# Optimization experiments

Hardware: AMD Instinct MI355X
Metric: run time of the kernel (lower is better)

Reference implementation:

```python
import jax, jax.numpy as jnp
import numpy as np

N = 30000      # node_size / new_node_size
R = 1000       # rel_size
T = 300000     # triple_size (edges)
D = 128        # node_hid == rel_hid
B = 1024       # train pairs
NNZ = 600000   # nnz of ent_adj / rel_adj
DEPTH = 2
GAMMA = 3.0
EPS = 1e-12    # F.normalize eps


def setup_inputs():
    key = jax.random.key(0)
    ks = jax.random.split(key, 12)
    adj = jnp.stack([jax.random.randint(ks[0], (T,), 0, N),
                     jax.random.randint(ks[1], (T,), 0, N)]).astype(jnp.int64)
    # one relation per triple: row ids are 0..T-1, col ids are relation ids
    r_index = jnp.stack([jnp.arange(T),
                         jax.random.randint(ks[2], (T,), 0, R)]).astype(jnp.int64)
    r_val = jnp.ones((T,), jnp.float32)
    ent_adj = jnp.stack([jax.random.randint(ks[3], (NNZ,), 0, N),
                         jax.random.randint(ks[4], (NNZ,), 0, N)]).astype(jnp.int64)
    rel_adj = jnp.stack([jax.random.randint(ks[5], (NNZ,), 0, N),
                         jax.random.randint(ks[6], (NNZ,), 0, R)]).astype(jnp.int64)
    ent_emb = jax.random.normal(ks[7], (N, D), jnp.float32) * 0.05
    rel_emb = jax.random.normal(ks[8], (R, D), jnp.float32) * 0.05
    attn_e = jax.random.normal(ks[9], (DEPTH, D, 1), jnp.float32) * 0.1
    attn_r = jax.random.normal(ks[10], (DEPTH, D, 1), jnp.float32) * 0.1
    train_pairs = jax.random.randint(ks[11], (B, 2), 0, N).astype(jnp.int64)
    return dict(ent_emb=ent_emb, rel_emb=rel_emb, attn_e=attn_e, attn_r=attn_r,
                r_val=r_val, adj=adj, r_index=r_index, ent_adj=ent_adj,
                rel_adj=rel_adj, train_pairs=train_pairs)


def _segment_softmax(vals, seg, num):
    m = jax.ops.segment_max(vals, seg, num_segments=num)
    e = jnp.exp(vals - m[seg])
    s = jax.ops.segment_sum(e, seg, num_segments=num)
    return e / s[seg]


def _avg(adj, emb):
    # sparse softmax of an all-ones matrix over dim=1 == 1/deg per nonzero, then spmm
    row, col = adj[0], adj[1]
    deg = jax.ops.segment_sum(jnp.ones_like(row, emb.dtype), row, num_segments=N)
    return jax.ops.segment_sum(emb[col] / deg[row][:, None], row, num_segments=N)


def _gat(features, rel_emb, adj, r_index, r_val, kernels):
    features = jnp.tanh(features)
    outputs = [features]
    row, col = adj[0], adj[1]
    for l in range(DEPTH):
        # sparse [T,R] @ rel_emb  -> per-triple relation embedding
        tri_rel = jax.ops.segment_sum(r_val[:, None] * rel_emb[r_index[1]],
                                      r_index[0], num_segments=T)          # [T,D]
        tri_rel = tri_rel / jnp.maximum(
            jnp.linalg.norm(tri_rel, axis=1, keepdims=True), EPS)
        neighs = features[col]                                             # [T,D]
        neighs = neighs - 2.0 * jnp.sum(neighs * tri_rel, axis=1,
                                        keepdims=True) * tri_rel
        att = jnp.squeeze(tri_rel @ kernels[l], axis=-1)                   # [T]
        att = _segment_softmax(att, row, N)
        new_features = jax.ops.segment_sum(neighs * att[:, None], row,
                                           num_segments=N)
        features = jnp.tanh(new_features)
        outputs.append(features)
    return jnp.concatenate(outputs, axis=-1)  # [N, (DEPTH+1)*D]


def _align_loss(pairs, emb):
    l, r = pairs[:, 0], pairs[:, 1]
    l_emb, r_emb = emb[l], emb[r]
    pos = jnp.sum(jnp.square(l_emb - r_emb), axis=-1, keepdims=True)       # [B,1]

    def sqdist(A, Bm):
        return (jnp.sum(jnp.square(A), axis=1)[:, None]
                + jnp.sum(jnp.square(Bm), axis=1)[None, :]
                - 2.0 * A @ Bm.T)

    bi = jnp.arange(pairs.shape[0])
    mask = jnp.ones((pairs.shape[0], N), emb.dtype)
    mask = mask.at[bi, l].add(-1.0).at[bi, r].add(-1.0)  # 1 - onehot(l) - onehot(r)

    def norm_lse(loss):
        mu = jax.lax.stop_gradient(jnp.mean(loss, axis=-1, keepdims=True))
        sd = jax.lax.stop_gradient(jnp.std(loss, axis=-1, keepdims=True))
        loss = (loss - mu) / sd
        return jax.nn.logsumexp(20.0 * loss + 8.0, axis=-1)

    l_loss = norm_lse((pos - sqdist(l_emb, emb) + GAMMA) * mask)
    r_loss = norm_lse((pos - sqdist(r_emb, emb) + GAMMA) * mask)
    return jnp.mean(l_loss + r_loss)


def reference(ent_emb, rel_emb, attn_e, attn_r, r_val, adj, r_index,
              ent_adj, rel_adj, train_pairs):
    ent_feature = _avg(ent_adj, ent_emb)   # [N,D]
    rel_feature = _avg(rel_adj, rel_emb)   # [N,D]
    out_rel = _gat(rel_feature, rel_emb, adj, r_index, r_val, attn_r)
    out_ent = _gat(ent_feature, rel_emb, adj, r_index, r_val, attn_e)
    emb = jnp.concatenate([out_ent, out_rel], axis=-1)  # [N, 6*D]
    return _align_loss(train_pairs, emb)
```

## Files before the change

### kernel.cpp

```cpp
#include <hip/hip_runtime.h>
#include <math.h>

#define N_ENT 30000
#define R_REL 1000
#define T_EDGE 300000
#define B_PAIR 1024
#define NNZ_E 600000
#define GAMMAF 3.0f
#define EPSV 1e-12f
#define EMBD 768
#define NPAD 30720
#define NT128 240
#define PTILES 480
#define SCB 118

typedef _Float16 half8 __attribute__((ext_vector_type(8)));
typedef _Float16 half4v __attribute__((ext_vector_type(4)));
typedef _Float16 half2v __attribute__((ext_vector_type(2)));
typedef float f32x4 __attribute__((ext_vector_type(4)));

__device__ inline void gl_lds16(const _Float16* g, _Float16* l){
  __builtin_amdgcn_global_load_lds(
      (const __attribute__((address_space(1))) unsigned int*)g,
      (__attribute__((address_space(3))) unsigned int*)l, 16, 0, 0);
}

__device__ inline float waveRedSum(float v){
  #pragma unroll
  for(int m=32;m>=1;m>>=1) v += __shfl_xor(v, m, 64);
  return v;
}

__device__ inline float fast_tanh(float x){
  x = fminf(10.f, fmaxf(-10.f, x));
  float e = __expf(2.f*x);
  return (e-1.f)/(e+1.f);
}

__global__ __launch_bounds__(256) void k_prep(const float* __restrict__ ent, const float* __restrict__ rel,
      const float* __restrict__ ae, const float* __restrict__ ar,
      _Float16* ehE, _Float16* ehR, _Float16* Eh, _Float16* relnH, float* expdot,
      const int* __restrict__ rA, int* cA, const int* __restrict__ rE, int* cE,
      const int* __restrict__ rR, int* cR){
  int i = blockIdx.x*256 + threadIdx.x;
  if(i < N_ENT*128) ehE[i] = (_Float16)ent[i];
  if(i < R_REL*128) ehR[i] = (_Float16)rel[i];
  if(i < (NPAD-N_ENT)*EMBD) Eh[(size_t)N_ENT*EMBD + i] = (_Float16)0.f;
  if(i < T_EDGE) atomicAdd(&cA[rA[i]], 1);
  if(i < NNZ_E){ atomicAdd(&cE[rE[i]], 1); atomicAdd(&cR[rR[i]], 1); }
  int r = i >> 6;
  if(r < R_REL){
    int lane = i & 63;
    float2 v = *(const float2*)(rel + (size_t)r*128 + lane*2);
    float ss = waveRedSum(v.x*v.x + v.y*v.y);
    float nrm = fmaxf(sqrtf(ss), EPSV);
    float2 u; u.x = v.x/nrm; u.y = v.y/nrm;
    half2v uh = {(_Float16)u.x, (_Float16)u.y};
    *(half2v*)(relnH + (size_t)r*128 + lane*2) = uh;
    const float* ks[4] = {ae, ae+128, ar, ar+128};
    #pragma unroll
    for(int k=0;k<4;k++){
      float2 w = *(const float2*)(ks[k] + lane*2);
      float d = waveRedSum(u.x*w.x + u.y*w.y);
      if(lane==0) expdot[k*R_REL + r] = __expf(d);
    }
  }
}

__global__ __launch_bounds__(256) void k_scanA(const int* c0, const int* c1, const int* c2,
                                               int* s0, int* s1, int* s2, int* part){
  const int* cnt = blockIdx.y==0 ? c0 : (blockIdx.y==1 ? c1 : c2);
  int* start     = blockIdx.y==0 ? s0 : (blockIdx.y==1 ? s1 : s2);
  __shared__ int wsum[4];
  int i = blockIdx.x*256 + threadIdx.x;
  int lane = threadIdx.x & 63, wid = threadIdx.x >> 6;
  int v = (i < N_ENT) ? cnt[i] : 0;
  int x = v;
  #pragma unroll
  for(int off=1; off<64; off<<=1){ int t=__shfl_up(x,off,64); if(lane>=off) x+=t; }
  if(lane==63) wsum[wid] = x;
  __syncthreads();
  int woff = 0;
  #pragma unroll
  for(int k=0;k<3;k++) if(k < wid) woff += wsum[k];
  if(i < N_ENT) start[i] = woff + x - v;
  if(threadIdx.x == 255) part[blockIdx.y*SCB + blockIdx.x] = woff + x;
}

__global__ __launch_bounds__(256) void k_scanB(int* part, int* tots){
  int wid = threadIdx.x>>6, lane = threadIdx.x&63;
  if(wid >= 3) return;
  int base = wid*SCB;
  int v0 = part[base + lane];
  int i1 = 64 + lane;
  int v1 = (i1 < SCB) ? part[base + i1] : 0;
  int x0 = v0, x1 = v1;
  #pragma unroll
  for(int off=1; off<64; off<<=1){
    int t0=__shfl_up(x0,off,64), t1=__shfl_up(x1,off,64);
    if(lane>=off){ x0+=t0; x1+=t1; }
  }
  int t0 = __shfl(x0, 63, 64);
  int t1 = __shfl(x1, 63, 64);
  part[base + lane] = x0 - v0;
  if(i1 < SCB) part[base + i1] = t0 + x1 - v1;
  if(lane == 0) tots[wid] = t0 + t1;
}

__global__ __launch_bounds__(256) void k_scanC(int* s0, int* s1, int* s2,
                                               int* u0, int* u1, int* u2,
                                               const int* part, const int* tots){
  int y = blockIdx.y;
  int* start  = y==0 ? s0 : (y==1 ? s1 : s2);
  int* cursor = y==0 ? u0 : (y==1 ? u1 : u2);
  int i = blockIdx.x*256 + threadIdx.x;
  int off = part[y*SCB + blockIdx.x];
  if(i < N_ENT){ int v = start[i] + off; start[i] = v; cursor[i] = v; }
  if(i == 0) start[N_ENT] = tots[y];
}

__global__ __launch_bounds__(256) void k_scatter3(
      const int* __restrict__ rA, const int* __restrict__ cAj, const int* __restrict__ rid,
      int* uA, int* scolA, int* sridA,
      const int* __restrict__ rE, const int* __restrict__ cEj, int* uE, int* scolE,
      const int* __restrict__ rR, const int* __restrict__ cRj, int* uR, int* scolR){
  int e = blockIdx.x*256 + threadIdx.x;
  if(e < T_EDGE){
    int p = atomicAdd(&uA[rA[e]], 1);
    scolA[p] = cAj[e];
    sridA[p] = rid[e];
  }
  if(e < NNZ_E){
    int p = atomicAdd(&uE[rE[e]], 1);
    scolE[p] = cEj[e];
    int q = atomicAdd(&uR[rR[e]], 1);
    scolR[q] = cRj[e];
  }
}

__global__ __launch_bounds__(256) void k_avg2(const int* __restrict__ startE, const int* __restrict__ scolE,
                        const _Float16* __restrict__ srcE,
                        const int* __restrict__ startR, const int* __restrict__ scolR,
                        const _Float16* __restrict__ srcR,
                        _Float16* featC, _Float16* Eh){
  int which = blockIdx.y;
  const int* start = which? startR : startE;
  const int* scol  = which? scolR : scolE;
  const _Float16* src = which? srcR : srcE;
  int pairOff = which? 2 : 0;
  int coloff  = which? 384 : 0;
  int r = blockIdx.x*4 + (threadIdx.x>>6);
  int lane = threadIdx.x & 63;
  int s0 = start[r], s1 = start[r+1];
  float ax=0.f, ay=0.f;
  int e = s0;
  for(; e+1<s1; e+=2){
    int c0 = scol[e], c1 = scol[e+1];
    half2v v0 = *(const half2v*)(src + (size_t)c0*128 + lane*2);
    half2v v1 = *(const half2v*)(src + (size_t)c1*128 + lane*2);
    ax += (float)v0[0] + (float)v1[0]; ay += (float)v0[1] + (float)v1[1];
  }
  if(e<s1){
    int c0 = scol[e];
    half2v v0 = *(const half2v*)(src + (size_t)c0*128 + lane*2);
    ax += (float)v0[0]; ay += (float)v0[1];
  }
  float inv = (s1>s0) ? 1.0f/(float)(s1-s0) : 0.f;
  float vx = fast_tanh(ax*inv), vy = fast_tanh(ay*inv);
  half2v hv = {(_Float16)vx, (_Float16)vy};
  *(half2v*)(featC + (size_t)r*256 + lane*4 + pairOff) = hv;
  *(half2v*)(Eh + (size_t)r*EMBD + coloff + lane*2) = hv;
}

__global__ __launch_bounds__(256) void k_edge2(const int* __restrict__ start, const int* __restrict__ scol,
      const int* __restrict__ srid, const _Float16* __restrict__ relnH,
      const float* __restrict__ expE, const float* __restrict__ expR,
      const _Float16* __restrict__ featIn, _Float16* featOut, _Float16* Eh, int colEnt, int colRel){
  int r = blockIdx.x*4 + (threadIdx.x>>6);
  int lane = threadIdx.x & 63;
  int s0 = start[r], s1 = start[r+1];
  float aEx=0,aEy=0,aRx=0,aRy=0, swE=0, swR=0;
  int e = s0;
  for(; e+1<s1; e+=2){
    int c0=scol[e], q0=srid[e], c1=scol[e+1], q1=srid[e+1];
    float wE0=expE[q0], wR0=expR[q0], wE1=expE[q1], wR1=expR[q1];
    half2v u0h = *(const half2v*)(relnH + (size_t)q0*128 + lane*2);
    half2v u1h = *(const half2v*)(relnH + (size_t)q1*128 + lane*2);
    half4v h0 = *(const half4v*)(featIn + (size_t)c0*256 + lane*4);
    half4v h1 = *(const half4v*)(featIn + (size_t)c1*256 + lane*4);
    float u0x=(float)u0h[0], u0y=(float)u0h[1], u1x=(float)u1h[0], u1y=(float)u1h[1];
    float e0x=(float)h0[0], e0y=(float)h0[1], r0x=(float)h0[2], r0y=(float)h0[3];
    float e1x=(float)h1[0], e1y=(float)h1[1], r1x=(float)h1[2], r1y=(float)h1[3];
    float d0 = e0x*u0x + e0y*u0y;
    float d1 = r0x*u0x + r0y*u0y;
    float d2 = e1x*u1x + e1y*u1y;
    float d3 = r1x*u1x + r1y*u1y;
    #pragma unroll
    for(int m=32;m>=1;m>>=1){
      d0 += __shfl_xor(d0,m,64); d1 += __shfl_xor(d1,m,64);
      d2 += __shfl_xor(d2,m,64); d3 += __shfl_xor(d3,m,64);
    }
    aEx += wE0*(e0x - 2.f*d0*u0x) + wE1*(e1x - 2.f*d2*u1x);
    aEy += wE0*(e0y - 2.f*d0*u0y) + wE1*(e1y - 2.f*d2*u1y);
    aRx += wR0*(r0x - 2.f*d1*u0x) + wR1*(r1x - 2.f*d3*u1x);
    aRy += wR0*(r0y - 2.f*d1*u0y) + wR1*(r1y - 2.f*d3*u1y);
    swE += wE0+wE1; swR += wR0+wR1;
  }
  if(e<s1){
    int c0=scol[e], q0=srid[e];
    float wE0=expE[q0], wR0=expR[q0];
    half2v u0h = *(const half2v*)(relnH + (size_t)q0*128 + lane*2);
    half4v h0 = *(const half4v*)(featIn + (size_t)c0*256 + lane*4);
    float u0x=(float)u0h[0], u0y=(float)u0h[1];
    float e0x=(float)h0[0], e0y=(float)h0[1], r0x=(float)h0[2], r0y=(float)h0[3];
    float d0 = e0x*u0x + e0y*u0y;
    float d1 = r0x*u0x + r0y*u0y;
    #pragma unroll
    for(int m=32;m>=1;m>>=1){ d0 += __shfl_xor(d0,m,64); d1 += __shfl_xor(d1,m,64); }
    aEx += wE0*(e0x - 2.f*d0*u0x);
    aEy += wE0*(e0y - 2.f*d0*u0y);
    aRx += wR0*(r0x - 2.f*d1*u0x);
    aRy += wR0*(r0y - 2.f*d1*u0y);
    swE += wE0; swR += wR0;
  }
  float iE = (s1>s0) ? 1.f/swE : 0.f;
  float iR = (s1>s0) ? 1.f/swR : 0.f;
  float vEx = fast_tanh(aEx*iE), vEy = fast_tanh(aEy*iE);
  float vRx = fast_tanh(aRx*iR), vRy = fast_tanh(aRy*iR);
  half4v ov = {(_Float16)vEx,(_Float16)vEy,(_Float16)vRx,(_Float16)vRy};
  *(half4v*)(featOut + (size_t)r*256 + lane*4) = ov;
  half2v he = {(_Float16)vEx,(_Float16)vEy};
  half2v hr = {(_Float16)vRx,(_Float16)vRy};
  *(half2v*)(Eh + (size_t)r*EMBD + colEnt + lane*2) = he;
  *(half2v*)(Eh + (size_t)r*EMBD + colRel + lane*2) = hr;
}

__global__ __launch_bounds__(256) void k_post(const _Float16* __restrict__ Eh, _Float16* embT,
      const int* __restrict__ tp, _Float16* Wh, float* cvec,
      float* qn, float* Svec, float* Pvec, float* QQ){
  __shared__ __align__(16) _Float16 til[64][72];
  __shared__ float sh0[256], sh1[256], sh2[256];
  int b = blockIdx.x;
  int tid = threadIdx.x;
  if(b < 5760){
    int r0 = (b % 480)*64, c0 = (b / 480)*64;
    int rr = tid>>3, c8 = (tid&7)*8;
    #pragma unroll
    for(int p=0;p<2;p++){
      int gr = r0 + rr + p*32;
      uint4 v = make_uint4(0u,0u,0u,0u);
      if(gr < N_ENT) v = *(const uint4*)(Eh + (size_t)gr*EMBD + c0 + c8);
      *(uint4*)&til[rr + p*32][c8] = v;
    }
    __syncthreads();
    #pragma unroll
    for(int p=0;p<2;p++){
      int cc = rr + p*32;
      __align__(16) _Float16 tmp[8];
      #pragma unroll
      for(int j=0;j<8;j++) tmp[j] = til[c8 + j][cc];
      *(uint4*)(embT + (size_t)(c0+cc)*NPAD + r0 + c8) = *(uint4*)tmp;
    }
  } else if(b < 5760 + B_PAIR){
    int i = b - 5760;
    int l = tp[2*i], r = tp[2*i+1];
    float sl=0.f, sr=0.f, sp=0.f;
    for(int c=tid;c<EMBD;c+=256){
      _Float16 lh = Eh[(size_t)l*EMBD+c], rh = Eh[(size_t)r*EMBD+c];
      float le = (float)lh, re = (float)rh;
      Wh[(size_t)i*EMBD+c]=lh; Wh[(size_t)(B_PAIR+i)*EMBD+c]=rh;
      sl += le*le; sr += re*re; float d = le-re; sp += d*d;
    }
    sh0[tid]=sl; sh1[tid]=sr; sh2[tid]=sp;
    __syncthreads();
    for(int w=128;w>0;w>>=1){
      if(tid<w){ sh0[tid]+=sh0[tid+w]; sh1[tid]+=sh1[tid+w]; sh2[tid]+=sh2[tid+w]; }
      __syncthreads();
    }
    if(tid==0){
      float pos = sh2[0];
      cvec[i]        = pos + GAMMAF - sh0[0];
      cvec[B_PAIR+i] = pos + GAMMAF - sh1[0];
    }
  } else {
    int wid = tid>>6, lane = tid&63;
    int gw = (b - 5760 - B_PAIR)*4 + wid;
    float s[12], p[12];
    #pragma unroll
    for(int q=0;q<12;q++){ s[q]=0.f; p[q]=0.f; }
    float q1=0.f, q2=0.f;
    for(int r=gw; r<NPAD; r+=960){
      if(r >= N_ENT){ if(lane==0) qn[r] = 1e30f; continue; }
      float v[12]; float ss=0.f;
      #pragma unroll
      for(int q=0;q<12;q++){ v[q] = (float)Eh[(size_t)r*EMBD + lane + 64*q]; ss += v[q]*v[q]; }
      ss = waveRedSum(ss);
      ss = __shfl(ss, 0, 64);
      if(lane==0){ qn[r] = ss; q1 += ss; q2 += ss*ss; }
      #pragma unroll
      for(int q=0;q<12;q++){ s[q] += v[q]; p[q] += ss*v[q]; }
    }
    #pragma unroll
    for(int q=0;q<12;q++){
      unsafeAtomicAdd(&Svec[lane + 64*q], s[q]);
      unsafeAtomicAdd(&Pvec[lane + 64*q], p[q]);
    }
    if(lane==0){ unsafeAtomicAdd(&QQ[0], q1); unsafeAtomicAdd(&QQ[1], q2); }
  }
}

__global__ __launch_bounds__(256) void k_syrk(const _Float16* __restrict__ embT, float* G){
  __shared__ __align__(16) _Float16 As[128*64];
  __shared__ __align__(16) _Float16 Bs[128*64];
  int id = blockIdx.x;
  int xcd = id & 7, rest = id >> 3;
  int kslc = xcd + 8*(rest/36);
  int tile = rest % 36;
  int m0 = (tile/6)*128, n0 = (tile%6)*128;
  int kbeg = kslc*1920, kend = kbeg + 1920;
  int tid = threadIdx.x;
  int w = tid>>6, lane = tid&63;
  int quad = lane>>4, l15 = lane&15;
  int lr = lane>>3, lc = lane&7;
  int wm = (w>>1)*64, wn = (w&1)*64;
  f32x4 acc[4][4];
  #pragma unroll
  for(int i=0;i<4;i++)
    #pragma unroll
    for(int j=0;j<4;j++) acc[i][j] = (f32x4){0.f,0.f,0.f,0.f};
  for(int k0=kbeg;k0<kend;k0+=64){
    #pragma unroll
    for(int p=0;p<4;p++){
      int r = p*32 + w*8 + lr;
      int cg = lc ^ (r&7);
      gl_lds16(embT + (size_t)(m0+r)*NPAD + k0 + cg*8, As + (p*32 + w*8)*64);
      gl_lds16(embT + (size_t)(n0+r)*NPAD + k0 + cg*8, Bs + (p*32 + w*8)*64);
    }
    __syncthreads();
    #pragma unroll
    for(int ks=0;ks<2;ks++){
      half8 af[4], bf[4];
      #pragma unroll
      for(int i=0;i<4;i++){
        int ml = wm + i*16 + l15;
        af[i] = *(half8*)(As + ml*64 + (((ks<<2)|quad) ^ (ml&7))*8);
      }
      #pragma unroll
      for(int j=0;j<4;j++){
        int nl = wn + j*16 + l15;
        bf[j] = *(half8*)(Bs + nl*64 + (((ks<<2)|quad) ^ (nl&7))*8);
      }
      #pragma unroll
      for(int i=0;i<4;i++)
        #pragma unroll
        for(int j=0;j<4;j++)
          acc[i][j] = __builtin_amdgcn_mfma_f32_16x16x32_f16(af[i], bf[j], acc[i][j], 0,0,0);
    }
    __syncthreads();
  }
  #pragma unroll
  for(int i=0;i<4;i++){
    #pragma unroll
    for(int r=0;r<4;r++){
      int m = m0 + wm + i*16 + quad*4 + r;
      #pragma unroll
      for(int j=0;j<4;j++){
        int n = n0 + wn + j*16 + l15;
        unsafeAtomicAdd(&G[(size_t)m*EMBD + n], acc[i][j][r]);
      }
    }
  }
}

__global__ __launch_bounds__(256) void k_gemmTh(const _Float16* __restrict__ Wh, const float* __restrict__ G,
                                                float* Tm){
  int tid = threadIdx.x, w = tid>>6, lane = tid&63;
  int quad = lane>>4, l15 = lane&15;
  int n0 = blockIdx.x*64;
  #pragma unroll
  for(int half=0; half<2; half++){
    int m0 = (blockIdx.y*8 + half*4 + w)*64;
    f32x4 acc[4][4];
    #pragma unroll
    for(int i=0;i<4;i++)
      #pragma unroll
      for(int j=0;j<4;j++) acc[i][j] = (f32x4){0.f,0.f,0.f,0.f};
    const _Float16* aB[4]; const float* bB[4];
    #pragma unroll
    for(int i=0;i<4;i++){
      aB[i] = Wh + (size_t)(m0+i*16+l15)*EMBD + quad*8;
      bB[i] = G  + (size_t)(n0+i*16+l15)*EMBD + quad*8;
    }
    for(int ks=0; ks<24; ks++){
      half8 af[4], bf[4];
      #pragma unroll
      for(int i=0;i<4;i++) af[i] = *(const half8*)(aB[i] + ks*32);
      #pragma unroll
      for(int j=0;j<4;j++){
        float4 f0 = *(const float4*)(bB[j] + ks*32);
        float4 f1 = *(const float4*)(bB[j] + ks*32 + 4);
        half8 h = {(_Float16)f0.x,(_Float16)f0.y,(_Float16)f0.z,(_Float16)f0.w,
                   (_Float16)f1.x,(_Float16)f1.y,(_Float16)f1.z,(_Float16)f1.w};
        bf[j] = h;
      }
      #pragma unroll
      for(int i=0;i<4;i++)
        #pragma unroll
        for(int j=0;j<4;j++)
          acc[i][j] = __builtin_amdgcn_mfma_f32_16x16x32_f16(af[i], bf[j], acc[i][j], 0,0,0);
    }
    #pragma unroll
    for(int i=0;i<4;i++)
      #pragma unroll
      for(int r=0;r<4;r++){
        int mg = m0 + i*16 + quad*4 + r;
        #pragma unroll
        for(int j=0;j<4;j++)
          Tm[(size_t)mg*EMBD + n0 + j*16 + l15] = acc[i][j][r];
      }
  }
}

__global__ __launch_bounds__(256) void k_rowstats(const _Float16* __restrict__ Wh, const float* __restrict__ Tm,
      const _Float16* __restrict__ Eh, const float* __restrict__ qn, const float* __restrict__ cvec,
      const int* __restrict__ tp, const float* __restrict__ Svec, const float* __restrict__ Pvec,
      const float* __restrict__ QQ, float* alpha, float* betav){
  int row = blockIdx.x*4 + (threadIdx.x>>6);
  int lane = threadIdx.x & 63;
  if(row >= 2*B_PAIR) return;
  int pi = row & (B_PAIR-1);
  int lp = tp[2*pi], rp = tp[2*pi+1];
  float d1=0,d2=0,d3=0,dl=0,dr=0;
  #pragma unroll
  for(int k=0;k<12;k++){
    int d = lane + 64*k;
    float a = (float)Wh[(size_t)row*EMBD + d];
    d1 += a*Svec[d];
    d2 += a*Pvec[d];
    d3 += a*Tm[(size_t)row*EMBD + d];
    dl += a*(float)Eh[(size_t)lp*EMBD + d];
    dr += a*(float)Eh[(size_t)rp*EMBD + d];
  }
  d1=waveRedSum(d1); d2=waveRedSum(d2); d3=waveRedSum(d3);
  dl=waveRedSum(dl); dr=waveRedSum(dr);
  if(lane==0){
    double c = (double)cvec[row], Q = (double)QQ[0], Q2 = (double)QQ[1], Nn = (double)N_ENT;
    double su  = Nn*c - Q + 2.0*(double)d1;
    double su2 = Nn*c*c - 2.0*c*Q + Q2 + 4.0*(c*(double)d1 - (double)d2) + 4.0*(double)d3;
    double ul = c - (double)qn[lp] + 2.0*(double)dl;
    double ur = c - (double)qn[rp] + 2.0*(double)dr;
    su -= ul + ur;
    if(lp != rp) su2 -= ul*ul + ur*ur;
    double mu = su/Nn;
    double var = su2/Nn - mu*mu;
    double sd = sqrt(fmax(var, 0.0));
    double al = 20.0/sd;
    alpha[row] = (float)al;
    betav[row] = (float)(8.0 - al*mu);
  }
}

__device__ inline void lseMerge(float& mx, float& sm, float om, float os){
  if(om > mx){ sm = sm*expf(mx-om) + os; mx = om; }
  else if(om != -INFINITY){ sm += os*expf(om-mx); }
}

__global__ __launch_bounds__(256,3) void k_gemmB(const _Float16* __restrict__ Wh, const _Float16* __restrict__ Eh,
    const float* __restrict__ cvec, const float* __restrict__ qn, const int* __restrict__ tp,
    const float* __restrict__ alpha, const float* __restrict__ betav, float* pm, float* ps){
  __shared__ __align__(16) _Float16 As[128*64];
  __shared__ __align__(16) _Float16 Bs[128*64];
  int id = blockIdx.x;
  int ntile = (id & 7) + ((id >> 7) << 3);
  int m0 = ((id >> 3) & 15) * 128;
  int n0 = ntile * 128;
  int tid = threadIdx.x;
  int w = tid>>6, lane = tid&63;
  int quad = lane>>4, l15 = lane&15;
  int lr = lane>>3, lc = lane&7;
  int wm = (w&1)*64, wn = (w>>1)*64;
  f32x4 acc[4][4];
  #pragma unroll
  for(int i=0;i<4;i++)
    #pragma unroll
    for(int j=0;j<4;j++) acc[i][j] = (f32x4){0.f,0.f,0.f,0.f};
  for(int k0=0;k0<EMBD;k0+=64){
    #pragma unroll
    for(int p=0;p<4;p++){
      int r = p*32 + w*8 + lr;
      int cg = lc ^ (r&7);
      gl_lds16(Wh + (size_t)(m0+r)*EMBD + k0 + cg*8, As + (p*32 + w*8)*64);
      gl_lds16(Eh + (size_t)(n0+r)*EMBD + k0 + cg*8, Bs + (p*32 + w*8)*64);
    }
    __syncthreads();
    #pragma unroll
    for(int ks=0;ks<2;ks++){
      half8 af[4], bf[4];
      #pragma unroll
      for(int i=0;i<4;i++){
        int ml = wm + i*16 + l15;
        af[i] = *(half8*)(As + ml*64 + (((ks<<2)|quad) ^ (ml&7))*8);
      }
      #pragma unroll
      for(int j=0;j<4;j++){
        int nl = wn + j*16 + l15;
        bf[j] = *(half8*)(Bs + nl*64 + (((ks<<2)|quad) ^ (nl&7))*8);
      }
      #pragma unroll
      for(int i=0;i<4;i++)
        #pragma unroll
        for(int j=0;j<4;j++)
          acc[i][j] = __builtin_amdgcn_mfma_f32_16x16x32_f16(af[i], bf[j], acc[i][j], 0,0,0);
    }
    __syncthreads();
  }
  float qv[4]; int jv[4];
  #pragma unroll
  for(int j=0;j<4;j++){ jv[j] = n0 + wn + j*16 + l15; qv[j] = qn[jv[j]]; }
  int ptile = ntile*2 + (w>>1);
  #pragma unroll
  for(int i=0;i<4;i++){
    int mbase = m0 + wm + i*16 + quad*4;
    #pragma unroll
    for(int r=0;r<4;r++){
      int mg = mbase + r;
      int pi = mg & (B_PAIR-1);
      int lp = tp[2*pi], rp = tp[2*pi+1];
      float cv = cvec[mg], al = alpha[mg], be = betav[mg];
      float mx = -INFINITY, sm = 0.f;
      #pragma unroll
      for(int j=0;j<4;j++){
        float u = fmaf(2.f, acc[i][j][r], cv - qv[j]);
        float z = fmaf(al, u, be);
        if(jv[j]==lp || jv[j]==rp) z = (lp==rp) ? fmaf(-al, u, be) : be;
        if(z > mx){ sm = sm*__expf(mx - z) + 1.f; mx = z; }
        else sm += __expf(z - mx);
      }
      #pragma unroll
      for(int m=8;m>=1;m>>=1){
        float om = __shfl_xor(mx, m, 64), os = __shfl_xor(sm, m, 64);
        lseMerge(mx, sm, om, os);
      }
      if(l15==0){ pm[(size_t)mg*PTILES + ptile] = mx; ps[(size_t)mg*PTILES + ptile] = sm; }
    }
  }
}

__global__ __launch_bounds__(256) void k_lse2(const float* __restrict__ pm, const float* __restrict__ ps,
                        float* accum, int* done, float* out){
  __shared__ float shm[256], shs[256];
  int row = blockIdx.x, tid = threadIdx.x;
  float mx = -INFINITY, sm = 0.f;
  for(int t=tid;t<PTILES;t+=256) lseMerge(mx, sm, pm[(size_t)row*PTILES+t], ps[(size_t)row*PTILES+t]);
  shm[tid]=mx; shs[tid]=sm;
  __syncthreads();
  for(int w=128;w>0;w>>=1){
    if(tid<w){
      float m2=shm[tid], s2=shs[tid];
      lseMerge(m2, s2, shm[tid+w], shs[tid+w]);
      shm[tid]=m2; shs[tid]=s2;
    }
    __syncthreads();
  }
  if(tid==0){
    float l = shm[0] + logf(shs[0]);
    atomicAdd(accum, l);
    __threadfence();
    int t = atomicAdd(done, 1);
    if(t == 2*B_PAIR - 1){
      __threadfence();
      float total = atomicAdd(accum, 0.0f);
      out[0] = total / (float)B_PAIR;
    }
  }
}

extern "C" void kernel_launch(void* const* d_in, const int* in_sizes, int n_in,
                              void* d_out, int out_size, void* d_ws, size_t ws_size,
                              hipStream_t stream) {
  const float* ent_emb = (const float*)d_in[0];
  const float* rel_emb = (const float*)d_in[1];
  const float* attn_e  = (const float*)d_in[2];
  const float* attn_r  = (const float*)d_in[3];
  const int* adj     = (const int*)d_in[5];
  const int* r_index = (const int*)d_in[6];
  const int* ent_adj = (const int*)d_in[7];
  const int* rel_adj = (const int*)d_in[8];
  const int* tp      = (const int*)d_in[9];
  float* out = (float*)d_out;

  const int* adj_row = adj;
  const int* adj_col = adj + T_EDGE;
  const int* rid1    = r_index + T_EDGE;

  char* base = (char*)d_ws;
  size_t off = 0;
  auto A = [&](size_t b)->void*{ void* p = base + off; off = (off + b + 255) & ~(size_t)255; return p; };
  int*   cntA  = (int*)  A((size_t)N_ENT*4);
  int*   cntE  = (int*)  A((size_t)N_ENT*4);
  int*   cntR  = (int*)  A((size_t)N_ENT*4);
  float* G     = (float*)A((size_t)EMBD*EMBD*4);
  float* Svec  = (float*)A(EMBD*4);
  float* Pvec  = (float*)A(EMBD*4);
  float* QQ    = (float*)A(2*4);
  float* accum = (float*)A(4);
  int*   done  = (int*)  A(4);
  size_t zero_end = off;
  int* startA = (int*)A((size_t)(N_ENT+1)*4);
  int* startE = (int*)A((size_t)(N_ENT+1)*4);
  int* startR = (int*)A((size_t)(N_ENT+1)*4);
  int* curA   = (int*)A((size_t)N_ENT*4);
  int* curE   = (int*)A((size_t)N_ENT*4);
  int* curR   = (int*)A((size_t)N_ENT*4);
  int* part   = (int*)A(3*SCB*4);
  int* tots   = (int*)A(3*4);
  int* scolA  = (int*)A((size_t)T_EDGE*4);
  int* sridA  = (int*)A((size_t)T_EDGE*4);
  int* scolE  = (int*)A((size_t)NNZ_E*4);
  int* scolR  = (int*)A((size_t)NNZ_E*4);
  _Float16* Eh = (_Float16*)A((size_t)NPAD*EMBD*2);
  char* X = (char*)A((size_t)EMBD*NPAD*2);
  _Float16* featC0 = (_Float16*)X;
  _Float16* featC1 = (_Float16*)(X + 16u*1024u*1024u);
  _Float16* embT   = (_Float16*)X;
  float*    pm     = (float*)X;
  float*    ps     = (float*)(X + 8u*1024u*1024u);
  _Float16* relnH  = (_Float16*)A((size_t)R_REL*128*2);
  _Float16* ehE   = (_Float16*)A((size_t)N_ENT*128*2);
  _Float16* ehR   = (_Float16*)A((size_t)R_REL*128*2);
  float* expdot  = (float*)A(4*R_REL*4);
  _Float16* Wh   = (_Float16*)A((size_t)2*B_PAIR*EMBD*2);
  float* Tm      = (float*)A((size_t)2*B_PAIR*EMBD*4);
  float* cvec    = (float*)A(2*B_PAIR*4);
  float* qn      = (float*)A((size_t)NPAD*4);
  float* alpha   = (float*)A(2*B_PAIR*4);
  float* betav   = (float*)A(2*B_PAIR*4);
  (void)ws_size; (void)in_sizes; (void)n_in; (void)out_size;

  hipMemsetAsync(d_ws, 0, zero_end, stream);

  k_prep<<<(N_ENT*128+255)/256, 256, 0, stream>>>(ent_emb, rel_emb, attn_e, attn_r,
                                                  ehE, ehR, Eh, relnH, expdot,
                                                  adj_row, cntA, ent_adj, cntE, rel_adj, cntR);

  dim3 gsa(SCB, 3);
  k_scanA<<<gsa, 256, 0, stream>>>(cntA, cntE, cntR, startA, startE, startR, part);
  k_scanB<<<1, 256, 0, stream>>>(part, tots);
  k_scanC<<<gsa, 256, 0, stream>>>(startA, startE, startR, curA, curE, curR, part, tots);
  k_scatter3<<<(NNZ_E+255)/256, 256, 0, stream>>>(adj_row, adj_col, rid1, curA, scolA, sridA,
                                                  ent_adj, ent_adj+NNZ_E, curE, scolE,
                                                  rel_adj, rel_adj+NNZ_E, curR, scolR);

  dim3 gavg(N_ENT/4, 2);
  k_avg2<<<gavg, 256, 0, stream>>>(startE, scolE, ehE, startR, scolR, ehR, featC0, Eh);
  k_edge2<<<N_ENT/4, 256, 0, stream>>>(startA, scolA, sridA, relnH, expdot + 0*R_REL, expdot + 2*R_REL,
                                       featC0, featC1, Eh, 128, 512);
  k_edge2<<<N_ENT/4, 256, 0, stream>>>(startA, scolA, sridA, relnH, expdot + 1*R_REL, expdot + 3*R_REL,
                                       featC1, featC0, Eh, 256, 640);

  k_post<<<5760 + B_PAIR + 240, 256, 0, stream>>>(Eh, embT, tp, Wh, cvec, qn, Svec, Pvec, QQ);

  k_syrk<<<576, 256, 0, stream>>>(embT, G);
  dim3 gT(EMBD/64, 4);
  k_gemmTh<<<gT, 256, 0, stream>>>(Wh, G, Tm);
  k_rowstats<<<2*B_PAIR/4, 256, 0, stream>>>(Wh, Tm, Eh, qn, cvec, tp, Svec, Pvec, QQ, alpha, betav);
  k_gemmB<<<NT128*16, 256, 0, stream>>>(Wh, Eh, cvec, qn, tp, alpha, betav, pm, ps);
  k_lse2<<<2*B_PAIR, 256, 0, stream>>>(pm, ps, accum, done, out);
}
```

Measured before the change: 882.2 us.

## Triple-buffer gemmB LDS tiles with 512-thread blocks and wider N tile

```diff
diff --git a/kernel.cpp b/kernel.cpp
--- a/kernel.cpp
+++ b/kernel.cpp
@@ -465,62 +465,100 @@
   else if(om != -INFINITY){ sm += os*expf(om-mx); }
 }
 
-__global__ __launch_bounds__(256,3) void k_gemmB(const _Float16* __restrict__ Wh, const _Float16* __restrict__ Eh,
+__device__ inline void stage_rows(const _Float16* __restrict__ src, _Float16* dstbase,
+                                  int p, int w, int lr, int lc){
+  int rb = p*64 + w*8;
+  int r = rb + lr;
+  int cg = lc ^ (r & 7);
+  gl_lds16(src + (size_t)r*EMBD + cg*8, dstbase + rb*64);
+}
+
+__global__ __launch_bounds__(512,2) void k_gemmB(const _Float16* __restrict__ Wh, const _Float16* __restrict__ Eh,
     const float* __restrict__ cvec, const float* __restrict__ qn, const int* __restrict__ tp,
     const float* __restrict__ alpha, const float* __restrict__ betav, float* pm, float* ps){
-  __shared__ __align__(16) _Float16 As[128*64];
-  __shared__ __align__(16) _Float16 Bs[128*64];
+  __shared__ __align__(16) _Float16 As[3*128*64];
+  __shared__ __align__(16) _Float16 Bs[3*256*64];
   int id = blockIdx.x;
   int ntile = (id & 7) + ((id >> 7) << 3);
   int m0 = ((id >> 3) & 15) * 128;
-  int n0 = ntile * 128;
+  int n0 = ntile * 256;
   int tid = threadIdx.x;
   int w = tid>>6, lane = tid&63;
   int quad = lane>>4, l15 = lane&15;
   int lr = lane>>3, lc = lane&7;
-  int wm = (w&1)*64, wn = (w>>1)*64;
+  int wr = w>>2, wc = w&3;
   f32x4 acc[4][4];
   #pragma unroll
   for(int i=0;i<4;i++)
     #pragma unroll
     for(int j=0;j<4;j++) acc[i][j] = (f32x4){0.f,0.f,0.f,0.f};
-  for(int k0=0;k0<EMBD;k0+=64){
-    #pragma unroll
-    for(int p=0;p<4;p++){
-      int r = p*32 + w*8 + lr;
-      int cg = lc ^ (r&7);
-      gl_lds16(Wh + (size_t)(m0+r)*EMBD + k0 + cg*8, As + (p*32 + w*8)*64);
-      gl_lds16(Eh + (size_t)(n0+r)*EMBD + k0 + cg*8, Bs + (p*32 + w*8)*64);
-    }
-    __syncthreads();
-    #pragma unroll
-    for(int ks=0;ks<2;ks++){
+  const _Float16* Abase = Wh + (size_t)m0*EMBD;
+  const _Float16* Bbase = Eh + (size_t)n0*EMBD;
+  #pragma unroll
+  for(int tt=0; tt<2; tt++){
+    stage_rows(Abase + tt*64, As + tt*(128*64), 0, w, lr, lc);
+    stage_rows(Abase + tt*64, As + tt*(128*64), 1, w, lr, lc);
+    #pragma unroll
+    for(int p=0;p<4;p++) stage_rows(Bbase + tt*64, Bs + tt*(256*64), p, w, lr, lc);
+  }
+  asm volatile("s_waitcnt vmcnt(6)" ::: "memory");
+  asm volatile("s_barrier" ::: "memory");
+  int s = 0;
+  for(int t=0; t<12; ++t){
+    _Float16* Acur = As + s*(128*64);
+    _Float16* Bcur = Bs + s*(256*64);
+    int sw = s+2; if(sw>=3) sw-=3;
+    _Float16* Anx = As + sw*(128*64);
+    _Float16* Bnx = Bs + sw*(256*64);
+    const _Float16* Asrc = Abase + (t+2)*64;
+    const _Float16* Bsrc = Bbase + (t+2)*64;
+    bool pre = (t < 10);
+    #pragma unroll
+    for(int ks=0; ks<2; ks++){
       half8 af[4], bf[4];
       #pragma unroll
       for(int i=0;i<4;i++){
-        int ml = wm + i*16 + l15;
-        af[i] = *(half8*)(As + ml*64 + (((ks<<2)|quad) ^ (ml&7))*8);
+        int ml = wr*64 + i*16 + l15;
+        af[i] = *(half8*)(Acur + ml*64 + (((ks<<2)|quad) ^ (ml&7))*8);
       }
       #pragma unroll
       for(int j=0;j<4;j++){
-        int nl = wn + j*16 + l15;
-        bf[j] = *(half8*)(Bs + nl*64 + (((ks<<2)|quad) ^ (nl&7))*8);
-      }
+        int nl = wc*64 + j*16 + l15;
+        bf[j] = *(half8*)(Bcur + nl*64 + (((ks<<2)|quad) ^ (nl&7))*8);
+      }
+      if(pre){
+        if(ks==0){
+          stage_rows(Asrc, Anx, 0, w, lr, lc);
+          stage_rows(Asrc, Anx, 1, w, lr, lc);
+          stage_rows(Bsrc, Bnx, 0, w, lr, lc);
+        } else {
+          stage_rows(Bsrc, Bnx, 1, w, lr, lc);
+          stage_rows(Bsrc, Bnx, 2, w, lr, lc);
+          stage_rows(Bsrc, Bnx, 3, w, lr, lc);
+        }
+      }
+      __builtin_amdgcn_s_setprio(1);
       #pragma unroll
       for(int i=0;i<4;i++)
         #pragma unroll
         for(int j=0;j<4;j++)
           acc[i][j] = __builtin_amdgcn_mfma_f32_16x16x32_f16(af[i], bf[j], acc[i][j], 0,0,0);
-    }
-    __syncthreads();
+      __builtin_amdgcn_s_setprio(0);
+      if(ks==1){
+        if(t < 10)       { asm volatile("s_waitcnt vmcnt(6)" ::: "memory"); }
+        else if(t == 10) { asm volatile("s_waitcnt vmcnt(0)" ::: "memory"); }
+      }
+      if(!(t==11 && ks==1)) asm volatile("s_barrier" ::: "memory");
+    }
+    s = s+1; if(s>=3) s=0;
   }
   float qv[4]; int jv[4];
   #pragma unroll
-  for(int j=0;j<4;j++){ jv[j] = n0 + wn + j*16 + l15; qv[j] = qn[jv[j]]; }
-  int ptile = ntile*2 + (w>>1);
+  for(int j=0;j<4;j++){ jv[j] = n0 + wc*64 + j*16 + l15; qv[j] = qn[jv[j]]; }
+  int ptile = ntile*4 + wc;
   #pragma unroll
   for(int i=0;i<4;i++){
-    int mbase = m0 + wm + i*16 + quad*4;
+    int mbase = m0 + wr*64 + i*16 + quad*4;
     #pragma unroll
     for(int r=0;r<4;r++){
       int mg = mbase + r;
@@ -664,6 +702,6 @@
   dim3 gT(EMBD/64, 4);
   k_gemmTh<<<gT, 256, 0, stream>>>(Wh, G, Tm);
   k_rowstats<<<2*B_PAIR/4, 256, 0, stream>>>(Wh, Tm, Eh, qn, cvec, tp, Svec, Pvec, QQ, alpha, betav);
-  k_gemmB<<<NT128*16, 256, 0, stream>>>(Wh, Eh, cvec, qn, tp, alpha, betav, pm, ps);
+  k_gemmB<<<1920, 512, 0, stream>>>(Wh, Eh, cvec, qn, tp, alpha, betav, pm, ps);
   k_lse2<<<2*B_PAIR, 256, 0, stream>>>(pm, ps, accum, done, out);
 }
```

Result: slower. 956.9 us (+8.5%).

## Rewrite score GEMM as 256x256 double-buffered tile with interleaved loads

Applied to the files above, without the earlier changes.

```diff
diff --git a/kernel.cpp b/kernel.cpp
--- a/kernel.cpp
+++ b/kernel.cpp
@@ -10,7 +10,6 @@
 #define EPSV 1e-12f
 #define EMBD 768
 #define NPAD 30720
-#define NT128 240
 #define PTILES 480
 #define SCB 118
 
@@ -465,62 +464,95 @@
   else if(om != -INFINITY){ sm += os*expf(om-mx); }
 }
 
-__global__ __launch_bounds__(256,3) void k_gemmB(const _Float16* __restrict__ Wh, const _Float16* __restrict__ Eh,
+__global__ __launch_bounds__(512,2) void k_gemmB(const _Float16* __restrict__ Wh, const _Float16* __restrict__ Eh,
     const float* __restrict__ cvec, const float* __restrict__ qn, const int* __restrict__ tp,
     const float* __restrict__ alpha, const float* __restrict__ betav, float* pm, float* ps){
-  __shared__ __align__(16) _Float16 As[128*64];
-  __shared__ __align__(16) _Float16 Bs[128*64];
+  __shared__ __align__(16) _Float16 As[2*256*64];
+  __shared__ __align__(16) _Float16 Bs[2*256*64];
   int id = blockIdx.x;
-  int ntile = (id & 7) + ((id >> 7) << 3);
-  int m0 = ((id >> 3) & 15) * 128;
-  int n0 = ntile * 128;
+  int xcd = id & 7, v = id >> 3;
+  int m0 = (v & 7) * 256;
+  int ntile = xcd + 8*(v >> 3);
+  int n0 = ntile * 256;
   int tid = threadIdx.x;
   int w = tid>>6, lane = tid&63;
   int quad = lane>>4, l15 = lane&15;
   int lr = lane>>3, lc = lane&7;
-  int wm = (w&1)*64, wn = (w>>1)*64;
-  f32x4 acc[4][4];
-  #pragma unroll
-  for(int i=0;i<4;i++)
+  int wr = w>>2, wc = w&3;
+  int g0 = quad ^ (l15&7);
+  int g1 = g0 ^ 4;
+  const _Float16* Ard = As + (size_t)(wr*128 + l15)*64;
+  const _Float16* Brd = Bs + (size_t)(wc*64  + l15)*64;
+  const _Float16* Asg = Wh + (size_t)(m0 + w*8 + lr)*EMBD + (lc^lr)*8;
+  const _Float16* Bsg = Eh + (size_t)(n0 + w*8 + lr)*EMBD + (lc^lr)*8;
+  _Float16* Asd = As + w*8*64;
+  _Float16* Bsd = Bs + w*8*64;
+  f32x4 acc[8][4];
+  #pragma unroll
+  for(int i=0;i<8;i++)
     #pragma unroll
     for(int j=0;j<4;j++) acc[i][j] = (f32x4){0.f,0.f,0.f,0.f};
-  for(int k0=0;k0<EMBD;k0+=64){
-    #pragma unroll
-    for(int p=0;p<4;p++){
-      int r = p*32 + w*8 + lr;
-      int cg = lc ^ (r&7);
-      gl_lds16(Wh + (size_t)(m0+r)*EMBD + k0 + cg*8, As + (p*32 + w*8)*64);
-      gl_lds16(Eh + (size_t)(n0+r)*EMBD + k0 + cg*8, Bs + (p*32 + w*8)*64);
-    }
-    __syncthreads();
-    #pragma unroll
-    for(int ks=0;ks<2;ks++){
-      half8 af[4], bf[4];
-      #pragma unroll
-      for(int i=0;i<4;i++){
-        int ml = wm + i*16 + l15;
-        af[i] = *(half8*)(As + ml*64 + (((ks<<2)|quad) ^ (ml&7))*8);
-      }
-      #pragma unroll
-      for(int j=0;j<4;j++){
-        int nl = wn + j*16 + l15;
-        bf[j] = *(half8*)(Bs + nl*64 + (((ks<<2)|quad) ^ (nl&7))*8);
-      }
-      #pragma unroll
-      for(int i=0;i<4;i++)
-        #pragma unroll
-        for(int j=0;j<4;j++)
-          acc[i][j] = __builtin_amdgcn_mfma_f32_16x16x32_f16(af[i], bf[j], acc[i][j], 0,0,0);
-    }
-    __syncthreads();
-  }
+  half8 bf[4][2], afc[2][2], afn[2][2];
+
+#define STA(b,kt,h) { const _Float16* s_ = Asg + (size_t)(h)*128*EMBD + (size_t)(kt)*64; \
+    _Float16* d_ = Asd + (b)*16384 + (h)*8192; \
+    gl_lds16(s_, d_); gl_lds16(s_ + (size_t)64*EMBD, d_ + 4096); }
+#define STB(b,kt,h) { const _Float16* s_ = Bsg + (size_t)(h)*128*EMBD + (size_t)(kt)*64; \
+    _Float16* d_ = Bsd + (b)*16384 + (h)*8192; \
+    gl_lds16(s_, d_); gl_lds16(s_ + (size_t)64*EMBD, d_ + 4096); }
+#define LDAQ(dst, b, q) { const _Float16* p_ = Ard + (b)*16384 + (q)*2048; \
+    dst[0][0] = *(const half8*)(p_ + g0*8); \
+    dst[0][1] = *(const half8*)(p_ + g1*8); \
+    dst[1][0] = *(const half8*)(p_ + 1024 + g0*8); \
+    dst[1][1] = *(const half8*)(p_ + 1024 + g1*8); }
+#define LDB(b) { const _Float16* p_ = Brd + (b)*16384; \
+    _Pragma("unroll") for(int j_=0;j_<4;j_++){ \
+      bf[j_][0] = *(const half8*)(p_ + j_*1024 + g0*8); \
+      bf[j_][1] = *(const half8*)(p_ + j_*1024 + g1*8); } }
+#define MM(q, AF) { _Pragma("unroll") for(int ks_=0;ks_<2;ks_++) \
+    _Pragma("unroll") for(int i_=0;i_<2;i_++) \
+    _Pragma("unroll") for(int j_=0;j_<4;j_++) \
+      acc[(q)*2+i_][j_] = __builtin_amdgcn_mfma_f32_16x16x32_f16(AF[i_][ks_], bf[j_][ks_], acc[(q)*2+i_][j_],0,0,0); }
+#define BARR asm volatile("s_barrier" ::: "memory")
+#define VMC6 asm volatile("s_waitcnt vmcnt(6)" ::: "memory")
+#define VMC0 asm volatile("s_waitcnt vmcnt(0)" ::: "memory")
+#define LGKW asm volatile("s_waitcnt lgkmcnt(0)" ::: "memory")
+#define PR1 __builtin_amdgcn_s_setprio(1)
+#define PR0 __builtin_amdgcn_s_setprio(0)
+#define KTILE(b, S1, S2, S3, S4, WEND) \
+    LDAQ(afc, b, 0); LDB(b); S1; BARR; \
+    PR1; MM(0, afc); PR0; BARR; \
+    LDAQ(afc, b, 1); S2; BARR; \
+    PR1; MM(1, afc); PR0; BARR; \
+    LDAQ(afc, b, 2); LDAQ(afn, b, 3); S3; BARR; \
+    PR1; MM(2, afc); PR0; LGKW; BARR; \
+    S4; BARR; \
+    PR1; MM(3, afn); PR0; WEND; BARR;
+
+  STB(0,0,0); STB(0,0,1); STA(0,0,0); STA(0,0,1);
+  STB(1,1,0); STB(1,1,1); STA(1,1,0);
+  VMC6; BARR;
+  #pragma unroll 1
+  for(int t=0; t<10; t+=2){
+    KTILE(0, STA(1,t+1,1), STB(0,t+2,0), STB(0,t+2,1), STA(0,t+2,0), VMC6);
+    KTILE(1, STA(0,t+2,1), STB(1,t+3,0), STB(1,t+3,1), STA(1,t+3,0), VMC6);
+  }
+  KTILE(0, STA(1,11,1), (void)0, (void)0, (void)0, VMC0);
+  KTILE(1, (void)0, (void)0, (void)0, (void)0, (void)0);
+#undef KTILE
+#undef STA
+#undef STB
+#undef LDAQ
+#undef LDB
+#undef MM
+
   float qv[4]; int jv[4];
   #pragma unroll
-  for(int j=0;j<4;j++){ jv[j] = n0 + wn + j*16 + l15; qv[j] = qn[jv[j]]; }
-  int ptile = ntile*2 + (w>>1);
-  #pragma unroll
-  for(int i=0;i<4;i++){
-    int mbase = m0 + wm + i*16 + quad*4;
+  for(int j=0;j<4;j++){ jv[j] = n0 + wc*64 + j*16 + l15; qv[j] = qn[jv[j]]; }
+  int ptile = ntile*4 + wc;
+  #pragma unroll
+  for(int ai=0;ai<8;ai++){
+    int mbase = m0 + wr*128 + ai*16 + quad*4;
     #pragma unroll
     for(int r=0;r<4;r++){
       int mg = mbase + r;
@@ -530,7 +562,7 @@
       float mx = -INFINITY, sm = 0.f;
       #pragma unroll
       for(int j=0;j<4;j++){
-        float u = fmaf(2.f, acc[i][j][r], cv - qv[j]);
+        float u = fmaf(2.f, acc[ai][j][r], cv - qv[j]);
         float z = fmaf(al, u, be);
         if(jv[j]==lp || jv[j]==rp) z = (lp==rp) ? fmaf(-al, u, be) : be;
         if(z > mx){ sm = sm*__expf(mx - z) + 1.f; mx = z; }
@@ -664,6 +696,6 @@
   dim3 gT(EMBD/64, 4);
   k_gemmTh<<<gT, 256, 0, stream>>>(Wh, G, Tm);
   k_rowstats<<<2*B_PAIR/4, 256, 0, stream>>>(Wh, Tm, Eh, qn, cvec, tp, Svec, Pvec, QQ, alpha, betav);
-  k_gemmB<<<NT128*16, 256, 0, stream>>>(Wh, Eh, cvec, qn, tp, alpha, betav, pm, ps);
+  k_gemmB<<<960, 512, 0, stream>>>(Wh, Eh, cvec, qn, tp, alpha, betav, pm, ps);
   k_lse2<<<2*B_PAIR, 256, 0, stream>>>(pm, ps, accum, done, out);
 }
```

Measured after the change: 1.258 ms. +42.5%, slower.
